# Performance work log

Hardware: AMD Instinct MI355X
Metric: run time of the kernel (lower is better)

## Reference

```python
import jax, jax.numpy as jnp
import numpy as np

B, N, E, F, U = 256, 240, 4338, 28, 100
NEG_SLOPE = 0.2  # PyG GATConv default negative_slope


def setup_inputs() -> dict:
    key = jax.random.key(0)
    ks = jax.random.split(key, 13)
    s = 0.05  # xavier-ish scale
    return {
        "inputs": jax.random.normal(ks[0], (B, N * F), jnp.float32),
        "state": jax.random.normal(ks[1], (B, N * U), jnp.float32),
        "edge_src": jax.random.randint(ks[2], (E,), 0, N, jnp.int32),
        "edge_dst": jax.random.randint(ks[3], (E,), 0, N, jnp.int32),
        # GATConv(U+F -> U): linear weight, attention vectors, output bias
        "Wg": jax.random.normal(ks[4], (U, U + F), jnp.float32) * s,
        "att_src": jax.random.normal(ks[5], (U,), jnp.float32) * s,
        "att_dst": jax.random.normal(ks[6], (U,), jnp.float32) * s,
        "gat_bias": jnp.zeros((U,), jnp.float32),
        # bias_1 added in _gc3 (self.biases[(100,)])
        "bias1": jnp.zeros((U,), jnp.float32),
        # GRU1: GRULinear(100, 200); GRU2: GRULinear(100, 100)
        "W_ru": jax.random.normal(ks[7], (U + F, 2 * U), jnp.float32) * s,
        "b_ru": jnp.zeros((2 * U,), jnp.float32),
        "W_c": jax.random.normal(ks[8], (U + F, U), jnp.float32) * s,
        "b_c": jnp.zeros((U,), jnp.float32),
    }


def _gat_gru(inputs, state, src, dst, Wg, att_src, att_dst, gat_bias, bias1,
             W_ru, b_ru, W_c, b_c):
    xi = inputs.reshape(B, N, F)
    xs = state.reshape(B, N, U)
    # _gc3: concat [state, inputs] -> GATConv per sample (vectorized here)
    x = jnp.concatenate([xs, xi], axis=2)                 # [B, N, U+F]
    h = jnp.einsum("bnf,cf->bnc", x, Wg)                  # [B, N, U]
    a_src = h @ att_src                                    # [B, N]
    a_dst = h @ att_dst                                    # [B, N]
    e = jax.nn.leaky_relu(a_src[:, src] + a_dst[:, dst], NEG_SLOPE)  # [B, E+N]
    eT = e.T                                               # [E+N, B]
    emax = jax.ops.segment_max(eT, dst, num_segments=N)    # [N, B]
    ex = jnp.exp(eT - emax[dst])
    denom = jax.ops.segment_sum(ex, dst, num_segments=N)   # [N, B]
    alpha = ex / denom[dst]                                # [E+N, B]
    msgs = h[:, src].transpose(1, 0, 2) * alpha[:, :, None]  # [E+N, B, U]
    agg = jax.ops.segment_sum(msgs, dst, num_segments=N)   # [N, B, U]
    gstate = agg.transpose(1, 0, 2) + gat_bias + bias1     # [B, N, U]
    st = gstate.reshape(B, N * U)
    # GRU gates (GRULinear concatenates [inputs, hidden] on feature dim)
    cat1 = jnp.concatenate([xi, gstate], axis=2).reshape(-1, U + F)
    ru = jax.nn.sigmoid((cat1 @ W_ru + b_ru).reshape(B, N, 2 * U))
    r = ru[..., :U].reshape(B, N * U)
    u = ru[..., U:].reshape(B, N * U)
    cat2 = jnp.concatenate([xi, (r * st).reshape(B, N, U)], axis=2).reshape(-1, U + F)
    c = jnp.tanh(cat2 @ W_c + b_c).reshape(B, N * U)
    return u * st + (1.0 - u) * c


def reference(inputs, state, edge_src, edge_dst, Wg, att_src, att_dst,
              gat_bias, bias1, W_ru, b_ru, W_c, b_c):
    # PyG GATConv default add_self_loops=True
    loops = jnp.arange(N, dtype=edge_src.dtype)
    src = jnp.concatenate([edge_src, loops])
    dst = jnp.concatenate([edge_dst, loops])
    return _gat_gru(inputs, state, src, dst, Wg, att_src, att_dst, gat_bias,
                    bias1, W_ru, b_ru, W_c, b_c)
```

## Files before the change

### kernel.cpp

```cpp
#include <hip/hip_runtime.h>

#define Bb 256
#define Nn 240
#define Ee 4338
#define Ff 28
#define Uu 100
#define Kk 128
#define ET (Ee + Nn)
#define AS 136

typedef __attribute__((ext_vector_type(8))) short bf16x8;
typedef __attribute__((ext_vector_type(4))) float f32x4;
typedef unsigned short u16;

__device__ __forceinline__ float bf2f(u16 u) {
  union { unsigned int i; float f; } v; v.i = ((unsigned int)u) << 16; return v.f;
}
__device__ __forceinline__ u16 f2bf(float f) {
  union { float ff; unsigned int i; } v; v.ff = f;
  unsigned int x = v.i;
  return (u16)((x + 0x7fffu + ((x >> 16) & 1u)) >> 16);
}
__device__ __forceinline__ void split4(const float4 v, ushort4& h, ushort4& l) {
  u16 h0 = f2bf(v.x), h1 = f2bf(v.y), h2 = f2bf(v.z), h3 = f2bf(v.w);
  h.x = h0; h.y = h1; h.z = h2; h.w = h3;
  l.x = f2bf(v.x - bf2f(h0)); l.y = f2bf(v.y - bf2f(h1));
  l.z = f2bf(v.z - bf2f(h2)); l.w = f2bf(v.w - bf2f(h3));
}
__device__ __forceinline__ bf16x8 pack8(ushort4 a, ushort4 b) {
  bf16x8 r;
  r[0] = (short)a.x; r[1] = (short)a.y; r[2] = (short)a.z; r[3] = (short)a.w;
  r[4] = (short)b.x; r[5] = (short)b.y; r[6] = (short)b.z; r[7] = (short)b.w;
  return r;
}

__global__ __launch_bounds__(512, 2) void k_fused(
    const float* __restrict__ stt, const float* __restrict__ inp,
    const float* __restrict__ Wg,
    const float* __restrict__ att_s, const float* __restrict__ att_d,
    const int* __restrict__ esrc, const int* __restrict__ edst,
    const float* __restrict__ gbias, const float* __restrict__ b1,
    const float* __restrict__ Wru, const float* __restrict__ bru,
    const float* __restrict__ Wc, const float* __restrict__ bc,
    float* __restrict__ out) {
  __shared__ float hbuf[Nn * Uu];
  __shared__ u16 ahL[32 * AS];
  __shared__ u16 alL[32 * AS];
  __shared__ float gch[32 * Uu];
  __shared__ u16 ugQ[32 * Uu];
  __shared__ float asrcL[Nn];
  __shared__ float adstL[Nn];
  __shared__ int coffL[Nn + 1];
  __shared__ int cslotL[ET];
  __shared__ int curL[Nn];
  __shared__ int cntA[Nn];

  int tid = threadIdx.x;
  int b = blockIdx.x;
  const size_t sbase = (size_t)b * Nn * Uu;
  const size_t ibase = (size_t)b * Nn * Ff;

  int w = tid >> 6, l = tid & 63, l15 = l & 15, q = l >> 4;
  int cw = w * 16 + l15;
  int llb = l & 31, half = l >> 5;

  f32x4 zero = {0.f, 0.f, 0.f, 0.f};

  auto stageChunk = [&](int c0, int rowsn, int base, int stride) {
    for (int j = base; j < rowsn * 32; j += stride) {
      int r = j >> 5, g = j & 31;
      float4 v = (g < 25)
          ? *(const float4*)(stt + sbase + (size_t)(c0 + r) * Uu + g * 4)
          : *(const float4*)(inp + ibase + (size_t)(c0 + r) * Ff + (g - 25) * 4);
      ushort4 hh, lo;
      split4(v, hh, lo);
      *(ushort4*)(ahL + r * AS + g * 4) = hh;
      *(ushort4*)(alL + r * AS + g * 4) = lo;
    }
  };

  {
    for (int i = tid; i < Nn; i += 512) { cntA[i] = 0; asrcL[i] = 0.f; adstL[i] = 0.f; }
    __syncthreads();

    for (int e = tid; e < Ee; e += 512) atomicAdd(&cntA[edst[e]], 1);
    bf16x8 wh[4], wl[4];
#pragma unroll
    for (int s = 0; s < 4; ++s) {
      float4 v0 = {0.f, 0.f, 0.f, 0.f}, v1 = {0.f, 0.f, 0.f, 0.f};
      if (cw < Uu) {
        v0 = *(const float4*)(Wg + cw * Kk + s * 32 + q * 8);
        v1 = *(const float4*)(Wg + cw * Kk + s * 32 + q * 8 + 4);
      }
      ushort4 h0, l0, h1, l1;
      split4(v0, h0, l0);
      split4(v1, h1, l1);
      wh[s] = pack8(h0, h1);
      wl[s] = pack8(l0, l1);
    }
    float av = (cw < Uu) ? att_s[cw] : 0.f;
    float dv = (cw < Uu) ? att_d[cw] : 0.f;
    __syncthreads();

    if (w == 0) {
      int carry = 0;
#pragma unroll
      for (int seg = 0; seg < 4; ++seg) {
        int idx = seg * 64 + l;
        int x = (idx < Nn) ? (cntA[idx] + 1) : 0;
        int v = x;
#pragma unroll
        for (int d = 1; d < 64; d <<= 1) {
          int t = __shfl_up(v, d, 64);
          if (l >= d) v += t;
        }
        if (idx < Nn) {
          int excl = carry + v - x;
          coffL[idx] = excl;
          curL[idx] = excl;
        }
        carry += __shfl(v, 63, 64);
      }
      if (l == 0) coffL[Nn] = carry;
    } else {
      stageChunk(0, 32, tid - 64, 448);
    }
    __syncthreads();

    for (int e = tid; e < Ee; e += 512) {
      int d = edst[e];
      cslotL[atomicAdd(&curL[d], 1)] = esrc[e];
    }
    for (int n = tid; n < Nn; n += 512) cslotL[atomicAdd(&curL[n], 1)] = n;

    for (int ch0 = 0; ch0 < Nn; ch0 += 32) {
      int rows = Nn - ch0; if (rows > 32) rows = 32;
      int nrt = rows >> 4;
      f32x4 acc[2]; acc[0] = zero; acc[1] = zero;
#pragma unroll
      for (int rt = 0; rt < 2; ++rt) if (rt < nrt) {
#pragma unroll
        for (int s = 0; s < 4; ++s) {
          bf16x8 a = *(const bf16x8*)(ahL + (rt * 16 + l15) * AS + s * 32 + q * 8);
          bf16x8 bb = *(const bf16x8*)(alL + (rt * 16 + l15) * AS + s * 32 + q * 8);
          acc[rt] = __builtin_amdgcn_mfma_f32_16x16x32_bf16(a, wh[s], acc[rt], 0, 0, 0);
          acc[rt] = __builtin_amdgcn_mfma_f32_16x16x32_bf16(bb, wh[s], acc[rt], 0, 0, 0);
          acc[rt] = __builtin_amdgcn_mfma_f32_16x16x32_bf16(a, wl[s], acc[rt], 0, 0, 0);
        }
      }
#pragma unroll
      for (int rt = 0; rt < 2; ++rt) if (rt < nrt) {
#pragma unroll
        for (int i = 0; i < 4; ++i) {
          float v = acc[rt][i];
          int row = rt * 16 + q * 4 + i;
          if (cw < Uu) hbuf[(ch0 + row) * Uu + cw] = v;
          float va = v * av, vd = v * dv;
#pragma unroll
          for (int msk = 1; msk < 16; msk <<= 1) {
            va += __shfl_xor(va, msk, 64);
            vd += __shfl_xor(vd, msk, 64);
          }
          if (l15 == 0) {
            atomicAdd(&asrcL[ch0 + row], va);
            atomicAdd(&adstL[ch0 + row], vd);
          }
        }
      }
      __syncthreads();
      int nx = ch0 + 32;
      if (nx < Nn) {
        int rowsn = Nn - nx; if (rowsn > 32) rowsn = 32;
        stageChunk(nx, rowsn, tid, 512);
      }
      __syncthreads();
    }
  }

  float4 gbv = {0.f, 0.f, 0.f, 0.f};
  if (l < 25) {
    int u0 = l * 4;
    gbv.x = gbias[u0 + 0] + b1[u0 + 0];
    gbv.y = gbias[u0 + 1] + b1[u0 + 1];
    gbv.z = gbias[u0 + 2] + b1[u0 + 2];
    gbv.w = gbias[u0 + 3] + b1[u0 + 3];
  }

  bf16x8 r0h[4], r0l[4], r1h[4], r1l[4], cch[4], ccl[4];
  int cw1 = 128 + cw;
#pragma unroll
  for (int s = 0; s < 4; ++s) {
    int kb = s * 32 + q * 8;
#pragma unroll
    for (int j = 0; j < 8; ++j) {
      int kp = kb + j;
      int k = (kp < Uu) ? (kp + Ff) : (kp - Uu);
      float v0 = Wru[k * (2 * Uu) + cw];
      u16 h0 = f2bf(v0);
      r0h[s][j] = (short)h0; r0l[s][j] = (short)f2bf(v0 - bf2f(h0));
      float v1 = (cw1 < 2 * Uu) ? Wru[k * (2 * Uu) + cw1] : 0.f;
      u16 h1 = f2bf(v1);
      r1h[s][j] = (short)h1; r1l[s][j] = (short)f2bf(v1 - bf2f(h1));
      float v2 = (cw < Uu) ? Wc[k * Uu + cw] : 0.f;
      u16 h2 = f2bf(v2);
      cch[s][j] = (short)h2; ccl[s][j] = (short)f2bf(v2 - bf2f(h2));
    }
  }
  float bru0 = bru[cw];
  float bru1 = (cw1 < 2 * Uu) ? bru[cw1] : 0.f;
  float bcv = (cw < Uu) ? bc[cw] : 0.f;

  for (int ch0 = 0; ch0 < Nn; ch0 += 32) {
    int rows = Nn - ch0; if (rows > 32) rows = 32;
    int nrt = rows >> 4;

    for (int n = ch0 + w; n < ch0 + rows; n += 8) {
      int o0 = coffL[n], deg = coffL[n + 1] - o0;
      float ad = adstL[n];
      float ax = 0.f, ay = 0.f, az = 0.f, aw2 = 0.f, den = 0.f;
      for (int c0 = 0; c0 < deg; c0 += 64) {
        int e = c0 + l;
        float we = 0.f; int s = 0;
        if (e < deg) {
          s = cslotL[o0 + e];
          float sc = asrcL[s] + ad;
          sc = (sc > 0.f) ? sc : 0.2f * sc;
          we = __expf(sc);
        }
        float d = we;
#pragma unroll
        for (int msk = 1; msk < 64; msk <<= 1) d += __shfl_xor(d, msk, 64);
        den += d;
        int cn = deg - c0; if (cn > 64) cn = 64;
        for (int e2 = 0; e2 < cn; e2 += 2) {
          int eh = e2 + half;
          float w2 = __shfl(we, eh, 64);
          int s2 = __shfl(s, eh, 64);
          if ((llb < 25) && eh < cn) {
            const float4 hv = *(const float4*)(hbuf + s2 * Uu + llb * 4);
            ax += w2 * hv.x; ay += w2 * hv.y; az += w2 * hv.z; aw2 += w2 * hv.w;
          }
        }
      }
      ax += __shfl_xor(ax, 32, 64);
      ay += __shfl_xor(ay, 32, 64);
      az += __shfl_xor(az, 32, 64);
      aw2 += __shfl_xor(aw2, 32, 64);
      if (l < 25) {
        float inv = 1.f / den;
        float4 o;
        o.x = ax * inv + gbv.x;
        o.y = ay * inv + gbv.y;
        o.z = az * inv + gbv.z;
        o.w = aw2 * inv + gbv.w;
        *(float4*)(gch + (n - ch0) * Uu + l * 4) = o;
      }
    }
    __syncthreads();

    for (int j = tid; j < rows * 32; j += 512) {
      int r = j >> 5, g = j & 31;
      float4 v = (g < 25)
          ? *(const float4*)(gch + r * Uu + g * 4)
          : *(const float4*)(inp + ibase + (size_t)(ch0 + r) * Ff + (g - 25) * 4);
      ushort4 hh, lo;
      split4(v, hh, lo);
      *(ushort4*)(ahL + r * AS + g * 4) = hh;
      *(ushort4*)(alL + r * AS + g * 4) = lo;
    }
    float sv[2][4];
#pragma unroll
    for (int rt = 0; rt < 2; ++rt) if (rt < nrt) {
#pragma unroll
      for (int i = 0; i < 4; ++i) {
        int row = rt * 16 + q * 4 + i;
        sv[rt][i] = (cw < Uu) ? gch[row * Uu + cw] : 0.f;
      }
    }
    __syncthreads();

    float pr[2][4];
    {
      f32x4 acc[2]; acc[0] = zero; acc[1] = zero;
#pragma unroll
      for (int rt = 0; rt < 2; ++rt) if (rt < nrt) {
#pragma unroll
        for (int s = 0; s < 4; ++s) {
          bf16x8 a = *(const bf16x8*)(ahL + (rt * 16 + l15) * AS + s * 32 + q * 8);
          bf16x8 bb = *(const bf16x8*)(alL + (rt * 16 + l15) * AS + s * 32 + q * 8);
          acc[rt] = __builtin_amdgcn_mfma_f32_16x16x32_bf16(a, r0h[s], acc[rt], 0, 0, 0);
          acc[rt] = __builtin_amdgcn_mfma_f32_16x16x32_bf16(bb, r0h[s], acc[rt], 0, 0, 0);
          acc[rt] = __builtin_amdgcn_mfma_f32_16x16x32_bf16(a, r0l[s], acc[rt], 0, 0, 0);
        }
      }
#pragma unroll
      for (int rt = 0; rt < 2; ++rt) if (rt < nrt) {
#pragma unroll
        for (int i = 0; i < 4; ++i) {
          int row = rt * 16 + q * 4 + i;
          float y = acc[rt][i] + bru0;
          float g = 1.f / (1.f + __expf(-y));
          if (cw < Uu) pr[rt][i] = g * sv[rt][i];
          else ugQ[row * Uu + (cw - Uu)] = (u16)(g * 65535.f + 0.5f);
        }
      }
    }
    {
      f32x4 acc[2]; acc[0] = zero; acc[1] = zero;
#pragma unroll
      for (int rt = 0; rt < 2; ++rt) if (rt < nrt) {
#pragma unroll
        for (int s = 0; s < 4; ++s) {
          bf16x8 a = *(const bf16x8*)(ahL + (rt * 16 + l15) * AS + s * 32 + q * 8);
          bf16x8 bb = *(const bf16x8*)(alL + (rt * 16 + l15) * AS + s * 32 + q * 8);
          acc[rt] = __builtin_amdgcn_mfma_f32_16x16x32_bf16(a, r1h[s], acc[rt], 0, 0, 0);
          acc[rt] = __builtin_amdgcn_mfma_f32_16x16x32_bf16(bb, r1h[s], acc[rt], 0, 0, 0);
          acc[rt] = __builtin_amdgcn_mfma_f32_16x16x32_bf16(a, r1l[s], acc[rt], 0, 0, 0);
        }
      }
#pragma unroll
      for (int rt = 0; rt < 2; ++rt) if (rt < nrt) {
#pragma unroll
        for (int i = 0; i < 4; ++i) {
          int row = rt * 16 + q * 4 + i;
          float y = acc[rt][i] + bru1;
          float g = 1.f / (1.f + __expf(-y));
          if (cw1 < 2 * Uu) ugQ[row * Uu + (cw1 - Uu)] = (u16)(g * 65535.f + 0.5f);
        }
      }
    }
    __syncthreads();

#pragma unroll
    for (int rt = 0; rt < 2; ++rt) if (rt < nrt) {
#pragma unroll
      for (int i = 0; i < 4; ++i) {
        int row = rt * 16 + q * 4 + i;
        if (cw < Uu) {
          float p = pr[rt][i];
          u16 hh = f2bf(p);
          ahL[row * AS + cw] = hh;
          alL[row * AS + cw] = f2bf(p - bf2f(hh));
        }
      }
    }
    __syncthreads();

    {
      f32x4 acc[2]; acc[0] = zero; acc[1] = zero;
#pragma unroll
      for (int rt = 0; rt < 2; ++rt) if (rt < nrt) {
#pragma unroll
        for (int s = 0; s < 4; ++s) {
          bf16x8 a = *(const bf16x8*)(ahL + (rt * 16 + l15) * AS + s * 32 + q * 8);
          bf16x8 bb = *(const bf16x8*)(alL + (rt * 16 + l15) * AS + s * 32 + q * 8);
          acc[rt] = __builtin_amdgcn_mfma_f32_16x16x32_bf16(a, cch[s], acc[rt], 0, 0, 0);
          acc[rt] = __builtin_amdgcn_mfma_f32_16x16x32_bf16(bb, cch[s], acc[rt], 0, 0, 0);
          acc[rt] = __builtin_amdgcn_mfma_f32_16x16x32_bf16(a, ccl[s], acc[rt], 0, 0, 0);
        }
      }
#pragma unroll
      for (int rt = 0; rt < 2; ++rt) if (rt < nrt) {
#pragma unroll
        for (int i = 0; i < 4; ++i) {
          int row = rt * 16 + q * 4 + i;
          if (cw < Uu) {
            float y = acc[rt][i] + bcv;
            float cv = 1.f - 2.f / (__expf(2.f * y) + 1.f);
            float u = (float)ugQ[row * Uu + cw] * (1.f / 65535.f);
            out[sbase + (size_t)(ch0 + row) * Uu + cw] = u * sv[rt][i] + (1.f - u) * cv;
          }
        }
      }
    }
  }
}

extern "C" void kernel_launch(void* const* d_in, const int* in_sizes, int n_in,
                              void* d_out, int out_size, void* d_ws, size_t ws_size,
                              hipStream_t stream) {
  const float* inp   = (const float*)d_in[0];
  const float* stt   = (const float*)d_in[1];
  const int*   esrc  = (const int*)d_in[2];
  const int*   edst  = (const int*)d_in[3];
  const float* Wg    = (const float*)d_in[4];
  const float* att_s = (const float*)d_in[5];
  const float* att_d = (const float*)d_in[6];
  const float* gbias = (const float*)d_in[7];
  const float* b1    = (const float*)d_in[8];
  const float* Wru   = (const float*)d_in[9];
  const float* bru   = (const float*)d_in[10];
  const float* Wc    = (const float*)d_in[11];
  const float* bc    = (const float*)d_in[12];
  float* out = (float*)d_out;

  k_fused<<<Bb, 512, 0, stream>>>(stt, inp, Wg, att_s, att_d, esrc, edst,
                                  gbias, b1, Wru, bru, Wc, bc, out);
}
```

Before: 218.0 us.

## Replace CSR gather aggregation with dense attention-matrix MFMA GEMM

Drops the CSR build (count, scan, scatter into slots) and the per-edge gather loop over the h buffer. For each 32-row chunk of destination nodes it now builds a dense 32x240 matrix of edge multiplicities using packed 8-bit shared-memory counters, turns it into unnormalised softmax weights, and aggregates with split-bf16 MFMA against a transposed h. The attention projections are folded into two extra columns of the Wg GEMM by precomputing Wg^T·att. Shared memory is reorganised into one manually aliased buffer. The cost is a dense 240-wide GEMM per chunk, an edge-list rescan per chunk, and the 8-bit counters overflow if more than 255 edges share one (dst, src) pair.

```diff
diff --git a/kernel.cpp b/kernel.cpp
--- a/kernel.cpp
+++ b/kernel.cpp
@@ -6,8 +6,8 @@
 #define Ff 28
 #define Uu 100
 #define Kk 128
-#define ET (Ee + Nn)
 #define AS 136
+#define KP 248
 
 typedef __attribute__((ext_vector_type(8))) short bf16x8;
 typedef __attribute__((ext_vector_type(4))) float f32x4;
@@ -27,12 +27,6 @@
   l.x = f2bf(v.x - bf2f(h0)); l.y = f2bf(v.y - bf2f(h1));
   l.z = f2bf(v.z - bf2f(h2)); l.w = f2bf(v.w - bf2f(h3));
 }
-__device__ __forceinline__ bf16x8 pack8(ushort4 a, ushort4 b) {
-  bf16x8 r;
-  r[0] = (short)a.x; r[1] = (short)a.y; r[2] = (short)a.z; r[3] = (short)a.w;
-  r[4] = (short)b.x; r[5] = (short)b.y; r[6] = (short)b.z; r[7] = (short)b.w;
-  return r;
-}
 
 __global__ __launch_bounds__(512, 2) void k_fused(
     const float* __restrict__ stt, const float* __restrict__ inp,
@@ -43,17 +37,22 @@
     const float* __restrict__ Wru, const float* __restrict__ bru,
     const float* __restrict__ Wc, const float* __restrict__ bc,
     float* __restrict__ out) {
-  __shared__ float hbuf[Nn * Uu];
-  __shared__ u16 ahL[32 * AS];
-  __shared__ u16 alL[32 * AS];
-  __shared__ float gch[32 * Uu];
-  __shared__ u16 ugQ[32 * Uu];
-  __shared__ float asrcL[Nn];
-  __shared__ float adstL[Nn];
-  __shared__ int coffL[Nn + 1];
-  __shared__ int cslotL[ET];
-  __shared__ int curL[Nn];
-  __shared__ int cntA[Nn];
+  __shared__ __align__(16) char smem[154752];
+  u16*      hTH    = (u16*)(smem);
+  u16*      hTL    = (u16*)(smem + 49600);
+  u16*      panel  = (u16*)(smem + 99200);
+  u16*      ahL    = panel;
+  u16*      alL    = panel + 32 * AS;
+  u16*      alphaL = panel;
+  float*    gch    = (float*)(smem + 116608);
+  unsigned* cntW   = (unsigned*)(smem + 116608);
+  u16*      alphaH = (u16*)(smem + 129408);
+  u16*      ugQ    = (u16*)(smem + 145280);
+  float*    asrcL  = (float*)(smem + 151680);
+  float*    adstL  = (float*)(smem + 152640);
+  float*    denC   = (float*)(smem + 153600);
+  float*    w_asL  = (float*)(smem + 153728);
+  float*    w_adL  = (float*)(smem + 154240);
 
   int tid = threadIdx.x;
   int b = blockIdx.x;
@@ -62,9 +61,9 @@
 
   int w = tid >> 6, l = tid & 63, l15 = l & 15, q = l >> 4;
   int cw = w * 16 + l15;
-  int llb = l & 31, half = l >> 5;
 
   f32x4 zero = {0.f, 0.f, 0.f, 0.f};
+  bf16x8 z8 = {0, 0, 0, 0, 0, 0, 0, 0};
 
   auto stageChunk = [&](int c0, int rowsn, int base, int stride) {
     for (int j = base; j < rowsn * 32; j += stride) {
@@ -79,59 +78,32 @@
     }
   };
 
+  if (tid < 256) {
+    int k = tid & 127;
+    const float* av = (tid < 128) ? att_s : att_d;
+    float acc = 0.f;
+    for (int c = 0; c < Uu; ++c) acc += Wg[c * Kk + k] * av[c];
+    ((tid < 128) ? w_asL : w_adL)[k] = acc;
+  } else {
+    stageChunk(0, 32, tid - 256, 256);
+  }
+  __syncthreads();
+
   {
-    for (int i = tid; i < Nn; i += 512) { cntA[i] = 0; asrcL[i] = 0.f; adstL[i] = 0.f; }
-    __syncthreads();
-
-    for (int e = tid; e < Ee; e += 512) atomicAdd(&cntA[edst[e]], 1);
     bf16x8 wh[4], wl[4];
 #pragma unroll
     for (int s = 0; s < 4; ++s) {
-      float4 v0 = {0.f, 0.f, 0.f, 0.f}, v1 = {0.f, 0.f, 0.f, 0.f};
-      if (cw < Uu) {
-        v0 = *(const float4*)(Wg + cw * Kk + s * 32 + q * 8);
-        v1 = *(const float4*)(Wg + cw * Kk + s * 32 + q * 8 + 4);
-      }
-      ushort4 h0, l0, h1, l1;
-      split4(v0, h0, l0);
-      split4(v1, h1, l1);
-      wh[s] = pack8(h0, h1);
-      wl[s] = pack8(l0, l1);
-    }
-    float av = (cw < Uu) ? att_s[cw] : 0.f;
-    float dv = (cw < Uu) ? att_d[cw] : 0.f;
-    __syncthreads();
-
-    if (w == 0) {
-      int carry = 0;
-#pragma unroll
-      for (int seg = 0; seg < 4; ++seg) {
-        int idx = seg * 64 + l;
-        int x = (idx < Nn) ? (cntA[idx] + 1) : 0;
-        int v = x;
-#pragma unroll
-        for (int d = 1; d < 64; d <<= 1) {
-          int t = __shfl_up(v, d, 64);
-          if (l >= d) v += t;
-        }
-        if (idx < Nn) {
-          int excl = carry + v - x;
-          coffL[idx] = excl;
-          curL[idx] = excl;
-        }
-        carry += __shfl(v, 63, 64);
-      }
-      if (l == 0) coffL[Nn] = carry;
-    } else {
-      stageChunk(0, 32, tid - 64, 448);
-    }
-    __syncthreads();
-
-    for (int e = tid; e < Ee; e += 512) {
-      int d = edst[e];
-      cslotL[atomicAdd(&curL[d], 1)] = esrc[e];
-    }
-    for (int n = tid; n < Nn; n += 512) cslotL[atomicAdd(&curL[n], 1)] = n;
+#pragma unroll
+      for (int j = 0; j < 8; ++j) {
+        int kp = s * 32 + q * 8 + j;
+        float v = (cw < Uu) ? Wg[cw * Kk + kp]
+                : (cw == Uu) ? w_asL[kp]
+                : (cw == Uu + 1) ? w_adL[kp] : 0.f;
+        u16 hh = f2bf(v);
+        wh[s][j] = (short)hh;
+        wl[s][j] = (short)f2bf(v - bf2f(hh));
+      }
+    }
 
     for (int ch0 = 0; ch0 < Nn; ch0 += 32) {
       int rows = Nn - ch0; if (rows > 32) rows = 32;
@@ -153,17 +125,15 @@
 #pragma unroll
         for (int i = 0; i < 4; ++i) {
           float v = acc[rt][i];
-          int row = rt * 16 + q * 4 + i;
-          if (cw < Uu) hbuf[(ch0 + row) * Uu + cw] = v;
-          float va = v * av, vd = v * dv;
-#pragma unroll
-          for (int msk = 1; msk < 16; msk <<= 1) {
-            va += __shfl_xor(va, msk, 64);
-            vd += __shfl_xor(vd, msk, 64);
-          }
-          if (l15 == 0) {
-            atomicAdd(&asrcL[ch0 + row], va);
-            atomicAdd(&adstL[ch0 + row], vd);
+          int krow = ch0 + rt * 16 + q * 4 + i;
+          if (cw < Uu) {
+            u16 hh = f2bf(v);
+            hTH[cw * KP + krow] = hh;
+            hTL[cw * KP + krow] = f2bf(v - bf2f(hh));
+          } else if (cw == Uu) {
+            asrcL[krow] = v;
+          } else if (cw == Uu + 1) {
+            adstL[krow] = v;
           }
         }
       }
@@ -175,15 +145,6 @@
       }
       __syncthreads();
     }
-  }
-
-  float4 gbv = {0.f, 0.f, 0.f, 0.f};
-  if (l < 25) {
-    int u0 = l * 4;
-    gbv.x = gbias[u0 + 0] + b1[u0 + 0];
-    gbv.y = gbias[u0 + 1] + b1[u0 + 1];
-    gbv.z = gbias[u0 + 2] + b1[u0 + 2];
-    gbv.w = gbias[u0 + 3] + b1[u0 + 3];
   }
 
   bf16x8 r0h[4], r0l[4], r1h[4], r1l[4], cch[4], ccl[4];
@@ -209,51 +170,94 @@
   float bru0 = bru[cw];
   float bru1 = (cw1 < 2 * Uu) ? bru[cw1] : 0.f;
   float bcv = (cw < Uu) ? bc[cw] : 0.f;
+  int n0 = (w >> 1) * 16 + l15;
+  int n1 = (4 + (w >> 1)) * 16 + l15;
+  float gb0 = (n0 < Uu) ? gbias[n0] + b1[n0] : 0.f;
+  float gb1 = (n1 < Uu) ? gbias[n1] + b1[n1] : 0.f;
 
   for (int ch0 = 0; ch0 < Nn; ch0 += 32) {
     int rows = Nn - ch0; if (rows > 32) rows = 32;
     int nrt = rows >> 4;
 
-    for (int n = ch0 + w; n < ch0 + rows; n += 8) {
-      int o0 = coffL[n], deg = coffL[n + 1] - o0;
-      float ad = adstL[n];
-      float ax = 0.f, ay = 0.f, az = 0.f, aw2 = 0.f, den = 0.f;
-      for (int c0 = 0; c0 < deg; c0 += 64) {
-        int e = c0 + l;
-        float we = 0.f; int s = 0;
-        if (e < deg) {
-          s = cslotL[o0 + e];
-          float sc = asrcL[s] + ad;
-          sc = (sc > 0.f) ? sc : 0.2f * sc;
-          we = __expf(sc);
-        }
-        float d = we;
-#pragma unroll
-        for (int msk = 1; msk < 64; msk <<= 1) d += __shfl_xor(d, msk, 64);
-        den += d;
-        int cn = deg - c0; if (cn > 64) cn = 64;
-        for (int e2 = 0; e2 < cn; e2 += 2) {
-          int eh = e2 + half;
-          float w2 = __shfl(we, eh, 64);
-          int s2 = __shfl(s, eh, 64);
-          if ((llb < 25) && eh < cn) {
-            const float4 hv = *(const float4*)(hbuf + s2 * Uu + llb * 4);
-            ax += w2 * hv.x; ay += w2 * hv.y; az += w2 * hv.z; aw2 += w2 * hv.w;
+    for (int i = tid; i < 32 * 62; i += 512) cntW[i] = 0;
+    __syncthreads();
+    for (int e = tid; e < Ee; e += 512) {
+      int d = edst[e];
+      unsigned r = (unsigned)(d - ch0);
+      if (r < 32u) {
+        int s = esrc[e];
+        atomicAdd(&cntW[r * 62 + (s >> 2)], 1u << (8 * (s & 3)));
+      }
+    }
+    if (tid < rows) {
+      int n = ch0 + tid;
+      atomicAdd(&cntW[tid * 62 + (n >> 2)], 1u << (8 * (n & 3)));
+    }
+    __syncthreads();
+    {
+      int d = tid >> 4, j = tid & 15;
+      int gd = ch0 + d;
+      float dsum = 0.f;
+      if (d < rows) {
+        float ad = adstL[gd];
+        for (int wi = j; wi < 62; wi += 16) {
+          unsigned c4 = cntW[d * 62 + wi];
+          ushort4 vh = {0, 0, 0, 0}, vl = {0, 0, 0, 0};
+          if (c4) {
+#pragma unroll
+            for (int bb = 0; bb < 4; ++bb) {
+              unsigned c = (c4 >> (8 * bb)) & 0xffu;
+              if (c) {
+                int s = wi * 4 + bb;
+                float sc = asrcL[s] + ad;
+                sc = (sc > 0.f) ? sc : 0.2f * sc;
+                float we = __expf(sc) * (float)c;
+                dsum += we;
+                u16 hh = f2bf(we);
+                ((u16*)&vh)[bb] = hh;
+                ((u16*)&vl)[bb] = f2bf(we - bf2f(hh));
+              }
+            }
           }
-        }
-      }
-      ax += __shfl_xor(ax, 32, 64);
-      ay += __shfl_xor(ay, 32, 64);
-      az += __shfl_xor(az, 32, 64);
-      aw2 += __shfl_xor(aw2, 32, 64);
-      if (l < 25) {
-        float inv = 1.f / den;
-        float4 o;
-        o.x = ax * inv + gbv.x;
-        o.y = ay * inv + gbv.y;
-        o.z = az * inv + gbv.z;
-        o.w = aw2 * inv + gbv.w;
-        *(float4*)(gch + (n - ch0) * Uu + l * 4) = o;
+          *(ushort4*)(alphaH + d * KP + wi * 4) = vh;
+          *(ushort4*)(alphaL + d * KP + wi * 4) = vl;
+        }
+      }
+      dsum += __shfl_xor(dsum, 1, 16);
+      dsum += __shfl_xor(dsum, 2, 16);
+      dsum += __shfl_xor(dsum, 4, 16);
+      dsum += __shfl_xor(dsum, 8, 16);
+      if (j == 0 && d < rows) denC[d] = 1.f / dsum;
+    }
+    __syncthreads();
+#pragma unroll
+    for (int p = 0; p < 2; ++p) {
+      int mh = w & 1, nt = p * 4 + (w >> 1);
+      if (nt > 6 || mh * 16 >= rows) continue;
+      int nn = p ? n1 : n0;
+      bool bv = (nn < Uu);
+      int arow = (mh * 16 + l15) * KP;
+      int brow = nn * KP;
+      f32x4 acc = zero;
+#pragma unroll
+      for (int s = 0; s < 8; ++s) {
+        int ko = s * 32 + q * 8;
+        bool kv = (s < 7) || (q < 2);
+        bf16x8 aH = kv ? *(const bf16x8*)(alphaH + arow + ko) : z8;
+        bf16x8 aL = kv ? *(const bf16x8*)(alphaL + arow + ko) : z8;
+        bf16x8 bH = (kv && bv) ? *(const bf16x8*)(hTH + brow + ko) : z8;
+        bf16x8 bL = (kv && bv) ? *(const bf16x8*)(hTL + brow + ko) : z8;
+        acc = __builtin_amdgcn_mfma_f32_16x16x32_bf16(aH, bH, acc, 0, 0, 0);
+        acc = __builtin_amdgcn_mfma_f32_16x16x32_bf16(aL, bH, acc, 0, 0, 0);
+        acc = __builtin_amdgcn_mfma_f32_16x16x32_bf16(aH, bL, acc, 0, 0, 0);
+      }
+      if (bv) {
+        float gb = p ? gb1 : gb0;
+#pragma unroll
+        for (int i = 0; i < 4; ++i) {
+          int m = mh * 16 + q * 4 + i;
+          gch[m * Uu + nn] = acc[i] * denC[m] + gb;
+        }
       }
     }
     __syncthreads();
@@ -373,6 +377,7 @@
         }
       }
     }
+    __syncthreads();
   }
 }
 
```

Measured after the change: 218.3 us. Within noise of the previous version (+0.2%).
